# Optimization experiments

Hardware: AMD Instinct MI355X
Metric: run time of the kernel (lower is better)

## Reference

```python
import jax, jax.numpy as jnp
import numpy as np

ENC_H, DEC_H, ATTN = 1024, 1024, 512
B, S = 32, 4096


def setup_inputs() -> dict:
    key = jax.random.key(0)
    k1, k2, k3, k4, k5, k6 = jax.random.split(key, 6)
    decoder_state = jax.random.normal(k1, (B, DEC_H), dtype=jnp.float32)
    encoder_outputs = jax.random.normal(k2, (B, S, ENC_H), dtype=jnp.float32)
    mask = jax.random.randint(k3, (B, S), 0, 2, dtype=jnp.int32)
    W_h = jax.random.normal(k4, (ENC_H, ATTN), dtype=jnp.float32) / np.sqrt(ENC_H)
    W_s = jax.random.normal(k5, (DEC_H, ATTN), dtype=jnp.float32) / np.sqrt(DEC_H)
    v = jax.random.normal(k6, (ATTN,), dtype=jnp.float32) / np.sqrt(ATTN)
    return {"decoder_state": decoder_state, "encoder_outputs": encoder_outputs,
            "mask": mask, "W_h": W_h, "W_s": W_s, "v": v}


def reference(decoder_state, encoder_outputs, mask, W_h, W_s, v):
    # proj_enc: (B, S, A), proj_dec: (B, 1, A)
    proj_enc = jnp.einsum('bse,ea->bsa', encoder_outputs, W_h)
    proj_dec = jnp.einsum('bd,da->ba', decoder_state, W_s)[:, None, :]
    # scores: (B, S) = v^T tanh(W_h h_j + W_s s_i)
    scores = jnp.einsum('bsa,a->bs', jnp.tanh(proj_enc + proj_dec), v)
    neg_inf = jnp.finfo(scores.dtype).min
    scores = jnp.where(mask == 0, neg_inf, scores)
    weights = jax.nn.softmax(scores, axis=-1)  # (B, S)
    context = jnp.einsum('bs,bse->be', weights, encoder_outputs)  # (B, ENC_H)
    return context, weights
```

## Files before the change

kernel.cpp:

```cpp
#include <hip/hip_runtime.h>
#include <hip/hip_bf16.h>
#include <float.h>
#include <math.h>

#define NB 32
#define NS 4096
#define NE 1024
#define ND 1024
#define NA 512

typedef __attribute__((ext_vector_type(4))) float f32x4;
typedef __attribute__((ext_vector_type(8))) short short8;
typedef __attribute__((address_space(3))) char lds_char_t;
typedef __attribute__((address_space(1))) const char g_char_t;

static __device__ __forceinline__ ushort f2bf(float f){
    union { float f; unsigned int u; } x; x.f = f;
    unsigned int u = x.u + 0x7fffu + ((x.u >> 16) & 1u);
    return (ushort)(u >> 16);
}

__global__ __launch_bounds__(256) void k_prep_wht(const float* __restrict__ Wh,
                                                  ushort* __restrict__ WT){
    int i = blockIdx.x * 256 + threadIdx.x;
    int k = i >> 9, a = i & 511;
    WT[a * 1024 + k] = f2bf(Wh[i]);
}

__global__ __launch_bounds__(512) void k_projdec(const float* __restrict__ dec,
                                                 const float* __restrict__ Ws,
                                                 float* __restrict__ pdp){
    int b = blockIdx.x >> 2, kc = blockIdx.x & 3;
    int a = threadIdx.x;
    const float* dp = dec + b * ND + kc * 256;
    const float* wp = Ws + (size_t)(kc * 256) * NA + a;
    float acc = 0.f;
    #pragma unroll 4
    for (int k = 0; k < 256; k++) acc += dp[k] * wp[(size_t)k * NA];
    pdp[(kc * NB + b) * NA + a] = acc;
}

__global__ __launch_bounds__(512, 4) void k_scores(const float* __restrict__ E,
                                                   const ushort* __restrict__ WT,
                                                   const float* __restrict__ pdp,
                                                   const float* __restrict__ v,
                                                   float* __restrict__ scores){
    const int t = threadIdx.x;
    const int wave = t >> 6, lane = t & 63;
    const int grp = lane >> 4, l15 = lane & 15;
    const int b = blockIdx.x >> 6;
    const int s0 = (blockIdx.x & 63) << 6;

    __shared__ __align__(16) float f32t[2][64 * 64];
    __shared__ float sc[64][8];

    const int c0 = wave * 128 + lane;
    const int c1 = c0 + 64;
    const int r0 = c0 >> 4, r1 = c1 >> 4;
    const int sd0 = (c0 & 15) ^ (r0 & 7);
    const int sd1 = (c1 & 15) ^ (r1 & 7);
    const float* g0 = E + ((size_t)(b * NS + s0 + r0)) * NE + sd0 * 4;
    const float* g1 = E + ((size_t)(b * NS + s0 + r1)) * NE + sd1 * 4;

    f32x4 acc[4][4];
    f32x4 zero; zero[0]=0.f; zero[1]=0.f; zero[2]=0.f; zero[3]=0.f;
    #pragma unroll
    for (int m = 0; m < 4; m++)
        #pragma unroll
        for (int n = 0; n < 4; n++) acc[m][n] = zero;

    auto dma = [&](int buf, int it){
        char* l0 = (char*)&f32t[buf][0] + c0 * 16;
        char* l1 = (char*)&f32t[buf][0] + c1 * 16;
        __builtin_amdgcn_global_load_lds((g_char_t*)(g0 + it * 64), (lds_char_t*)l0, 16, 0, 0);
        __builtin_amdgcn_global_load_lds((g_char_t*)(g1 + it * 64), (lds_char_t*)l1, 16, 0, 0);
    };

    dma(0, 0);

    const int cb = wave * 64 + l15;

    for (int it = 0; it < 16; ++it){
        __syncthreads();

        short8 wt[2][4];
        const ushort* wbase = WT + it * 64 + grp * 8;
        #pragma unroll
        for (int kk = 0; kk < 2; kk++)
            #pragma unroll
            for (int n = 0; n < 4; n++)
                wt[kk][n] = *(const short8*)(wbase + (size_t)(cb + n * 16) * 1024 + kk * 32);
        __builtin_amdgcn_sched_barrier(0);

        if (it < 15) dma((it + 1) & 1, it + 1);
        __builtin_amdgcn_sched_barrier(0);

        const char* base = (const char*)&f32t[it & 1][0];
        #pragma unroll
        for (int kk = 0; kk < 2; kk++){
            #pragma unroll
            for (int m = 0; m < 4; m++){
                const int r = m * 16 + l15;
                const int scg = kk * 8 + grp * 2;
                f32x4 lo = *(const f32x4*)(base + r * 256 + ((scg       ^ (r & 7)) << 4));
                f32x4 hi = *(const f32x4*)(base + r * 256 + (((scg + 1) ^ (r & 7)) << 4));
                short8 af;
                #pragma unroll
                for (int e = 0; e < 4; e++){
                    af[e]     = (short)__builtin_bit_cast(ushort, __float2bfloat16(lo[e]));
                    af[e + 4] = (short)__builtin_bit_cast(ushort, __float2bfloat16(hi[e]));
                }
                #pragma unroll
                for (int n = 0; n < 4; n++)
                    acc[m][n] = __builtin_amdgcn_mfma_f32_16x16x32_bf16(af, wt[kk][n], acc[m][n], 0, 0, 0);
            }
        }
    }

    float pdc[4], vc[4];
    #pragma unroll
    for (int n = 0; n < 4; n++){
        int c = wave * 64 + n * 16 + l15;
        float p = 0.f;
        #pragma unroll
        for (int kc = 0; kc < 4; kc++) p += pdp[(kc * NB + b) * NA + c];
        pdc[n] = p;
        vc[n] = v[c];
    }
    #pragma unroll
    for (int m = 0; m < 4; m++){
        #pragma unroll
        for (int j = 0; j < 4; j++){
            float s = 0.f;
            #pragma unroll
            for (int n = 0; n < 4; n++) s += tanhf(acc[m][n][j] + pdc[n]) * vc[n];
            s += __shfl_xor(s, 1);
            s += __shfl_xor(s, 2);
            s += __shfl_xor(s, 4);
            s += __shfl_xor(s, 8);
            if (l15 == 0) sc[m * 16 + grp * 4 + j][wave] = s;
        }
    }
    __syncthreads();
    if (t < 64){
        float s = 0.f;
        #pragma unroll
        for (int w = 0; w < 8; w++) s += sc[t][w];
        scores[b * NS + s0 + t] = s;
    }
}

__global__ __launch_bounds__(256) void k_softmax(const float* __restrict__ scores,
                                                 const int* __restrict__ mask,
                                                 float* __restrict__ weights){
    int b = blockIdx.x, t = threadIdx.x;
    __shared__ float red[8];
    float vals[16];
    float mx = -FLT_MAX;
    #pragma unroll
    for (int i = 0; i < 16; i++){
        int s = i * 256 + t;
        float x = scores[b * NS + s];
        x = (mask[b * NS + s] != 0) ? x : -FLT_MAX;
        vals[i] = x;
        mx = fmaxf(mx, x);
    }
    #pragma unroll
    for (int off = 32; off; off >>= 1) mx = fmaxf(mx, __shfl_xor(mx, off));
    int wv = t >> 6;
    if ((t & 63) == 0) red[wv] = mx;
    __syncthreads();
    mx = fmaxf(fmaxf(red[0], red[1]), fmaxf(red[2], red[3]));
    float sum = 0.f;
    #pragma unroll
    for (int i = 0; i < 16; i++){ vals[i] = __expf(vals[i] - mx); sum += vals[i]; }
    #pragma unroll
    for (int off = 32; off; off >>= 1) sum += __shfl_xor(sum, off);
    if ((t & 63) == 0) red[4 + wv] = sum;
    __syncthreads();
    sum = red[4] + red[5] + red[6] + red[7];
    float inv = 1.f / sum;
    #pragma unroll
    for (int i = 0; i < 16; i++) weights[b * NS + i * 256 + t] = vals[i] * inv;
}

__global__ __launch_bounds__(1024) void k_context(const float* __restrict__ E,
                                                  const float* __restrict__ weights,
                                                  float* __restrict__ part){
    int b = blockIdx.x >> 3, ch = blockIdx.x & 7;
    int t = threadIdx.x;
    int h = t >> 8, tg = t & 255;
    __shared__ float wsm[512];
    __shared__ __align__(16) f32x4 red[4][256];
    if (t < 512) wsm[t] = weights[b * NS + ch * 512 + t];
    __syncthreads();
    const f32x4* Ep = (const f32x4*)(E + ((size_t)b * NS + ch * 512 + h * 128) * NE) + tg;
    f32x4 acc; acc[0]=0.f; acc[1]=0.f; acc[2]=0.f; acc[3]=0.f;
    #pragma unroll 4
    for (int s = 0; s < 128; s++){
        f32x4 e = Ep[(size_t)s * 256];
        float w = wsm[h * 128 + s];
        acc[0] += w * e[0]; acc[1] += w * e[1];
        acc[2] += w * e[2]; acc[3] += w * e[3];
    }
    red[h][tg] = acc;
    __syncthreads();
    if (h == 0){
        f32x4 a0 = red[0][tg], a1 = red[1][tg], a2 = red[2][tg], a3 = red[3][tg];
        f32x4 s;
        s[0] = a0[0]+a1[0]+a2[0]+a3[0];
        s[1] = a0[1]+a1[1]+a2[1]+a3[1];
        s[2] = a0[2]+a1[2]+a2[2]+a3[2];
        s[3] = a0[3]+a1[3]+a2[3]+a3[3];
        *(f32x4*)(part + ((size_t)(b * 8 + ch)) * NE + tg * 4) = s;
    }
}

__global__ __launch_bounds__(256) void k_reduce_ctx(const float* __restrict__ part,
                                                    float* __restrict__ ctx){
    int i = blockIdx.x * 256 + threadIdx.x;
    int b = i >> 10, e = i & 1023;
    float s = 0.f;
    #pragma unroll
    for (int ch = 0; ch < 8; ch++) s += part[((size_t)(b * 8 + ch)) * NE + e];
    ctx[i] = s;
}

extern "C" void kernel_launch(void* const* d_in, const int* in_sizes, int n_in,
                              void* d_out, int out_size, void* d_ws, size_t ws_size,
                              hipStream_t stream){
    const float* dec  = (const float*)d_in[0];
    const float* E    = (const float*)d_in[1];
    const int*   mask = (const int*)d_in[2];
    const float* Wh   = (const float*)d_in[3];
    const float* Ws   = (const float*)d_in[4];
    const float* v    = (const float*)d_in[5];
    float* ctx = (float*)d_out;
    float* weights = (float*)d_out + NB * NE;

    char* ws = (char*)d_ws;
    ushort* WT   = (ushort*)ws;
    float*  part = (float*)ws;
    float*  pdp  = (float*)(ws + (1 << 20));
    float*  scr  = (float*)(ws + (1 << 20) + (256 << 10));

    k_prep_wht<<<2048, 256, 0, stream>>>(Wh, WT);
    k_projdec<<<128, 512, 0, stream>>>(dec, Ws, pdp);
    k_scores<<<2048, 512, 0, stream>>>(E, WT, pdp, v, scr);
    k_softmax<<<32, 256, 0, stream>>>(scr, mask, weights);
    k_context<<<256, 1024, 0, stream>>>(E, weights, part);
    k_reduce_ctx<<<128, 256, 0, stream>>>(part, ctx);
}
```

Baseline: 432.5 us.

## Stage encoder tiles through registers, converting to bf16 before LDS write

```diff
diff --git a/kernel.cpp b/kernel.cpp
--- a/kernel.cpp
+++ b/kernel.cpp
@@ -11,8 +11,7 @@
 
 typedef __attribute__((ext_vector_type(4))) float f32x4;
 typedef __attribute__((ext_vector_type(8))) short short8;
-typedef __attribute__((address_space(3))) char lds_char_t;
-typedef __attribute__((address_space(1))) const char g_char_t;
+typedef __attribute__((ext_vector_type(4))) short short4v;
 
 static __device__ __forceinline__ ushort f2bf(float f){
     union { float f; unsigned int u; } x; x.f = f;
@@ -51,16 +50,14 @@
     const int b = blockIdx.x >> 6;
     const int s0 = (blockIdx.x & 63) << 6;
 
-    __shared__ __align__(16) float f32t[2][64 * 64];
+    __shared__ __align__(16) ushort bft[2][64 * 64];
     __shared__ float sc[64][8];
 
-    const int c0 = wave * 128 + lane;
-    const int c1 = c0 + 64;
-    const int r0 = c0 >> 4, r1 = c1 >> 4;
-    const int sd0 = (c0 & 15) ^ (r0 & 7);
-    const int sd1 = (c1 & 15) ^ (r1 & 7);
-    const float* g0 = E + ((size_t)(b * NS + s0 + r0)) * NE + sd0 * 4;
-    const float* g1 = E + ((size_t)(b * NS + s0 + r1)) * NE + sd1 * 4;
+    const int sr = t >> 3, scg = t & 7;
+    const float* gsrc = E + ((size_t)(b * NS + s0 + sr)) * NE + scg * 8;
+    const unsigned swb = (unsigned)(sr * 128 + ((scg ^ (sr & 7)) << 4));
+
+    f32x4 stlo, sthi;
 
     f32x4 acc[4][4];
     f32x4 zero; zero[0]=0.f; zero[1]=0.f; zero[2]=0.f; zero[3]=0.f;
@@ -69,20 +66,28 @@
         #pragma unroll
         for (int n = 0; n < 4; n++) acc[m][n] = zero;
 
-    auto dma = [&](int buf, int it){
-        char* l0 = (char*)&f32t[buf][0] + c0 * 16;
-        char* l1 = (char*)&f32t[buf][0] + c1 * 16;
-        __builtin_amdgcn_global_load_lds((g_char_t*)(g0 + it * 64), (lds_char_t*)l0, 16, 0, 0);
-        __builtin_amdgcn_global_load_lds((g_char_t*)(g1 + it * 64), (lds_char_t*)l1, 16, 0, 0);
+    auto stage_load = [&](int it){
+        const f32x4* p = (const f32x4*)(gsrc + it * 64);
+        stlo = p[0]; sthi = p[1];
     };
-
-    dma(0, 0);
+    auto stage_write = [&](int buf){
+        short8 h;
+        #pragma unroll
+        for (int e = 0; e < 4; e++){
+            h[e]     = (short)f2bf(stlo[e]);
+            h[e + 4] = (short)f2bf(sthi[e]);
+        }
+        *(short8*)((char*)&bft[buf][0] + swb) = h;
+    };
 
     const int cb = wave * 64 + l15;
 
+    stage_load(0);
+    asm volatile("s_waitcnt vmcnt(0)" ::: "memory");
+    stage_write(0);
+    __builtin_amdgcn_s_barrier();
+
     for (int it = 0; it < 16; ++it){
-        __syncthreads();
-
         short8 wt[2][4];
         const ushort* wbase = WT + it * 64 + grp * 8;
         #pragma unroll
@@ -92,29 +97,29 @@
                 wt[kk][n] = *(const short8*)(wbase + (size_t)(cb + n * 16) * 1024 + kk * 32);
         __builtin_amdgcn_sched_barrier(0);
 
-        if (it < 15) dma((it + 1) & 1, it + 1);
+        if (it < 15) stage_load(it + 1);
         __builtin_amdgcn_sched_barrier(0);
 
-        const char* base = (const char*)&f32t[it & 1][0];
+        const char* base = (const char*)&bft[it & 1][0];
         #pragma unroll
         for (int kk = 0; kk < 2; kk++){
             #pragma unroll
             for (int m = 0; m < 4; m++){
                 const int r = m * 16 + l15;
-                const int scg = kk * 8 + grp * 2;
-                f32x4 lo = *(const f32x4*)(base + r * 256 + ((scg       ^ (r & 7)) << 4));
-                f32x4 hi = *(const f32x4*)(base + r * 256 + (((scg + 1) ^ (r & 7)) << 4));
-                short8 af;
-                #pragma unroll
-                for (int e = 0; e < 4; e++){
-                    af[e]     = (short)__builtin_bit_cast(ushort, __float2bfloat16(lo[e]));
-                    af[e + 4] = (short)__builtin_bit_cast(ushort, __float2bfloat16(hi[e]));
-                }
+                const int g = kk * 4 + grp;
+                short8 af = *(const short8*)(base + r * 128 + (((g ^ (r & 7)) << 4)));
                 #pragma unroll
                 for (int n = 0; n < 4; n++)
                     acc[m][n] = __builtin_amdgcn_mfma_f32_16x16x32_bf16(af, wt[kk][n], acc[m][n], 0, 0, 0);
             }
         }
+        __builtin_amdgcn_sched_barrier(0);
+
+        if (it < 15){
+            asm volatile("s_waitcnt vmcnt(0)" ::: "memory");
+            stage_write((it + 1) & 1);
+        }
+        __builtin_amdgcn_s_barrier();
     }
 
     float pdc[4], vc[4];
```

After: 413.3 us. 4.4% less time.
